# Kernel tuning notes

Measured on AMD Instinct MI355X. Metric: run time of the kernel, lower is better.

## Reference

```python
import jax, jax.numpy as jnp
import numpy as np

D_MODEL = 64
LN_EPS = 1e-5


def _conv1d(x, w, b, stride, pad):
    # x: (B, Cin, L), w: (Cout, Cin, K)
    y = jax.lax.conv_general_dilated(x, w, (stride,), [(pad, pad)],
                                     dimension_numbers=('NCH', 'OIH', 'NCH'))
    return y + b[None, :, None]


def _layernorm(x, g, b):
    # normalize over last dim (feature dim), matching nn.LayerNorm(d_model)
    m = jnp.mean(x, axis=-1, keepdims=True)
    v = jnp.var(x, axis=-1, keepdims=True)
    return (x - m) * jax.lax.rsqrt(v + LN_EPS) * g + b


def _pos_embed(L, d):
    pos = jnp.arange(L, dtype=jnp.float32)[:, None]
    div = jnp.exp(jnp.arange(0, d, 2, dtype=jnp.float32) * (-np.log(10000.0) / d))
    pe = jnp.zeros((L, d), jnp.float32)
    pe = pe.at[:, 0::2].set(jnp.sin(pos * div))
    pe = pe.at[:, 1::2].set(jnp.cos(pos * div))
    return pe


def setup_inputs():
    key = jax.random.key(0)
    ks = jax.random.split(key, 20)
    B, L, D = 128, 4096, D_MODEL
    G = D // 4  # 16 convs per kernel-size group (kernels cycle [3,5,7,9])
    inp = {'x': jax.random.normal(ks[0], (B, 1, L), jnp.float32)}
    kernels = [3, 5, 7, 9]
    for i, k in enumerate(kernels):
        fan = float(1.0 / np.sqrt(k))
        inp['tok_w%d' % k] = jax.random.uniform(ks[1 + 2 * i], (G, 1, k), jnp.float32, -fan, fan)
        inp['tok_b%d' % k] = jax.random.uniform(ks[2 + 2 * i], (G,), jnp.float32, -fan, fan)
    fan = float(1.0 / np.sqrt(D * 4))
    for j in range(3):
        inp['c_w%d' % (j + 1)] = jax.random.uniform(ks[10 + 2 * j], (D, D, 4), jnp.float32, -fan, fan)
        inp['c_b%d' % (j + 1)] = jax.random.uniform(ks[11 + 2 * j], (D,), jnp.float32, -fan, fan)
    for j in range(2):
        inp['ln_g%d' % (j + 1)] = jnp.ones((D,), jnp.float32)
        inp['ln_b%d' % (j + 1)] = jnp.zeros((D,), jnp.float32)
    return inp


def reference(x, tok_w3, tok_b3, tok_w5, tok_b5, tok_w7, tok_b7, tok_w9, tok_b9,
              c_w1, c_b1, c_w2, c_b2, c_w3, c_b3, ln_g1, ln_b1, ln_g2, ln_b2):
    B, _, L = x.shape
    D = D_MODEL
    # TokenEmbedding: conv i has kernel [3,5,7,9][i%4]; fuse the d_model 1-channel
    # convs into 4 grouped convs (one per kernel size), then interleave channels.
    outs = [
        _conv1d(x, tok_w3, tok_b3, 1, 1),
        _conv1d(x, tok_w5, tok_b5, 1, 2),
        _conv1d(x, tok_w7, tok_b7, 1, 3),
        _conv1d(x, tok_w9, tok_b9, 1, 4),
    ]  # each (B, D//4, L); group g holds channels i with i % 4 == g, ordered by i // 4
    emb = jnp.stack(outs, axis=2).reshape(B, D, L)  # channel i = (i//4)*4 + (i%4)
    # add sinusoidal positional embedding (dropout is identity in eval mode)
    h = emb + _pos_embed(L, D).T[None]  # (B, D, L)
    # CompressionEmbedding: conv(k=4, s=2, p=1) -> tanh -> LN (over D) chain
    h = jnp.tanh(_conv1d(h, c_w1, c_b1, 2, 1))
    h = _layernorm(h.transpose(0, 2, 1), ln_g1, ln_b1).transpose(0, 2, 1)
    h = jnp.tanh(_conv1d(h, c_w2, c_b2, 2, 1))
    h = _layernorm(h.transpose(0, 2, 1), ln_g2, ln_b2).transpose(0, 2, 1)
    h = jnp.tanh(_conv1d(h, c_w3, c_b3, 2, 1))
    return h.transpose(0, 2, 1)  # (B, L//8, D)
```

## Files before the change

kernel.cpp:

```cpp
#include <hip/hip_runtime.h>
#include <math.h>

#define BATCH 128
#define LN_EPS 1e-5f

typedef short bf16x8 __attribute__((ext_vector_type(8)));
typedef short bf16x4 __attribute__((ext_vector_type(4)));
typedef float f32x4  __attribute__((ext_vector_type(4)));

__device__ __forceinline__ ushort f2bf(float f) {
    return __builtin_bit_cast(ushort, (__bf16)f);
}

__device__ __forceinline__ float fast_tanh(float v) {
    float e = __expf(2.f * v);
    float r = __builtin_amdgcn_rcpf(e + 1.f);
    return fmaf(-2.f, r, 1.f);
}

__device__ __forceinline__ float fast_rsqrt(float v) {
    return __builtin_amdgcn_rsqf(v);
}

__global__ __launch_bounds__(256, 2)
void prep_kernel(const float* __restrict__ cw1, const float* __restrict__ cw2,
                 const float* __restrict__ cw3,
                 const float* __restrict__ w3, const float* __restrict__ b3,
                 const float* __restrict__ w5, const float* __restrict__ b5,
                 const float* __restrict__ w7, const float* __restrict__ b7,
                 const float* __restrict__ w9, const float* __restrict__ b9,
                 const float* __restrict__ cb1, const float* __restrict__ cb2,
                 const float* __restrict__ cb3,
                 const float* __restrict__ lg1, const float* __restrict__ lb1,
                 const float* __restrict__ lg2, const float* __restrict__ lb2,
                 ushort* __restrict__ Wm23, ushort* __restrict__ Wm1,
                 float* __restrict__ W0c, float* __restrict__ W3c,
                 float* __restrict__ pe1c,
                 float* __restrict__ cb2t, float* __restrict__ B2k0,
                 float* __restrict__ B2k3,
                 float* __restrict__ cb3t, float* __restrict__ B3k0,
                 float* __restrict__ B3k3) {
    const int tid = threadIdx.x;
    const int bx  = blockIdx.x;

    __shared__ float tile[64][12];
    __shared__ float red[4][64][24];

    if (tid < 64) {
        int idx = bx * 64 + tid;
        int s = idx >> 14, r = idx & 16383;
        int j = r & 7, l15 = (r >> 3) & 15, dt = (r >> 7) & 3;
        int quad = (r >> 9) & 3, k2 = (r >> 11) & 1, kk = (r >> 12) & 3;
        int dout = dt * 16 + l15, din = k2 * 32 + quad * 8 + j;
        const float* cw = (s == 0) ? cw2 : cw3;
        const float* lg = (s == 0) ? lg1 : lg2;
        Wm23[idx] = f2bf(cw[dout * 256 + din * 4 + kk] * lg[din]);
    }

    if (bx == 1 && tid < 128) {
        const int s = tid >> 6, ch = tid & 63;
        const float* cw = (s == 0) ? cw2 : cw3;
        const float* lb = (s == 0) ? lb1 : lb2;
        float full = 0.f, k0 = 0.f, k3 = 0.f;
        for (int din = 0; din < 64; ++din) {
            float bv = lb[din];
            const float* wr = cw + ch * 256 + din * 4;
            k0 = fmaf(wr[0], bv, k0);
            k3 = fmaf(wr[3], bv, k3);
            full = fmaf(wr[0] + wr[1] + wr[2] + wr[3], bv, full);
        }
        if (s == 0) { cb2t[ch] = cb2[ch] + full; B2k0[ch] = k0; B2k3[ch] = k3; }
        else        { cb3t[ch] = cb3[ch] + full; B3k0[ch] = k0; B3k3[ch] = k3; }
    }

    if (bx == 0) {
        const int ch = tid & 63, part = tid >> 6;
        const float* cw1row = cw1 + ch * 256;
        float acc[24];
#pragma unroll
        for (int j = 0; j < 24; ++j) acc[j] = 0.f;
        for (int din = part * 16; din < part * 16 + 16; ++din) {
            int ki = din & 3, g = din >> 2;
            float wl[9];
#pragma unroll
            for (int j = 0; j < 9; ++j) wl[j] = 0.f;
            if (ki == 0)      { for (int j = 0; j < 3; ++j) wl[3 + j] = w3[g * 3 + j]; }
            else if (ki == 1) { for (int j = 0; j < 5; ++j) wl[2 + j] = w5[g * 5 + j]; }
            else if (ki == 2) { for (int j = 0; j < 7; ++j) wl[1 + j] = w7[g * 7 + j]; }
            else              { for (int j = 0; j < 9; ++j) wl[j]     = w9[g * 9 + j]; }
#pragma unroll
            for (int kk = 0; kk < 4; ++kk) {
                float c = cw1row[din * 4 + kk];
#pragma unroll
                for (int u = 0; u < 9; ++u) acc[kk + u] += c * wl[u];
            }
            float c0 = cw1row[din * 4 + 0], c3 = cw1row[din * 4 + 3];
#pragma unroll
            for (int u = 0; u < 4; ++u) { acc[16 + u] += c0 * wl[5 + u]; acc[20 + u] += c3 * wl[u]; }
        }
#pragma unroll
        for (int j = 0; j < 24; ++j) red[part][ch][j] = acc[j];
    }

    for (int i = tid; i < 320; i += 256) {
        int d2 = i / 10, pp = i - d2 * 10;
        int p = 8 * bx - 1 + pp;
        int din0 = 2 * d2, g = d2 >> 1;
        float sv = 0.f, cv = 0.f;
        if (p >= 0 && p < 4096) {
            float dv = __expf((float)din0 * -0.14391156831212787f);
            float s, c;
            __sincosf((float)p * dv, &s, &c);
            bool lo = (din0 & 3) == 0;
            sv = s + (lo ? b3[g] : b7[g]);
            cv = c + (lo ? b5[g] : b9[g]);
        }
        tile[din0][pp] = sv;
        tile[din0 + 1][pp] = cv;
    }
    __syncthreads();

    if (bx == 0 && tid < 64) {
        const int ch = tid;
        float w24[24];
#pragma unroll
        for (int j = 0; j < 24; ++j)
            w24[j] = red[0][ch][j] + red[1][ch][j] + red[2][ch][j] + red[3][ch][j];
        int dt = ch >> 4, l15 = ch & 15;
#pragma unroll
        for (int quad = 0; quad < 4; ++quad)
#pragma unroll
            for (int j = 0; j < 8; ++j) {
                int k = quad * 8 + j;
                Wm1[((quad * 4 + dt) * 16 + l15) * 8 + j] = f2bf(k < 12 ? w24[k] : 0.f);
            }
#pragma unroll
        for (int u = 0; u < 4; ++u) { W0c[ch * 4 + u] = w24[16 + u]; W3c[ch * 4 + u] = w24[20 + u]; }
    }

    {
        const int ll = tid >> 6, ch = tid & 63;
        const int l = bx * 4 + ll;
        float acc = cb1[ch];
        const float* cwr = cw1 + ch * 256;
        for (int din = 0; din < 64; ++din) {
            float4 w = *(const float4*)(cwr + din * 4);
            acc = fmaf(w.x, tile[din][2 * ll + 0],
                  fmaf(w.y, tile[din][2 * ll + 1],
                  fmaf(w.z, tile[din][2 * ll + 2],
                  fmaf(w.w, tile[din][2 * ll + 3], acc))));
        }
        pe1c[(size_t)l * 64 + ch] = acc;
    }
}

__global__ __launch_bounds__(256, 2)
void mega_kernel(const float* __restrict__ x,
                 const ushort* __restrict__ Wm1, const ushort* __restrict__ Wm23,
                 const float* __restrict__ pe1c,
                 const float* __restrict__ W0c, const float* __restrict__ W3c,
                 const float* __restrict__ cb2t, const float* __restrict__ B2k0,
                 const float* __restrict__ B2k3,
                 const float* __restrict__ cb3t, const float* __restrict__ B3k0,
                 const float* __restrict__ B3k3,
                 float* __restrict__ out) {
    const int b0 = blockIdx.y;
    const int g0 = blockIdx.x * 32;
    const int tid = threadIdx.x;

    __shared__ __align__(16) ushort xs[2][320];
    __shared__ __align__(16) ushort TE1[2][68][72];
    __shared__ __align__(16) ushort TO1[2][68][72];
    __shared__ __align__(16) ushort TE2[2][34][72];
    __shared__ __align__(16) ushort TO2[2][34][72];

    for (int i = tid; i < 640; i += 256) {
        int ba = (i >= 320) ? 1 : 0, j = i - ba * 320;
        int g = 8 * g0 - 11 + j;
        float v = (g >= 0 && g < 4096) ? x[(size_t)(b0 + ba * 64) * 4096 + g] : 0.f;
        xs[ba][j] = f2bf(v);
    }
    __syncthreads();

    const int wv = tid >> 6, lane = tid & 63;
    const int quad = lane >> 4, l15 = lane & 15;

    {
        bf16x8 afr1[4];
#pragma unroll
        for (int dt = 0; dt < 4; ++dt)
            afr1[dt] = *(const bf16x8*)&Wm1[((quad * 4 + dt) * 16 + l15) * 8];
        const int qstart = 4 * g0 - 3;

        float4 pv[4];
        unsigned xA[4], xB[4];
        {
            const int m = wv * 16 + l15;
            const int q = qstart + m;
            const int qc = (q < 0) ? 0 : ((q > 2047) ? 2047 : q);
            const float* pb_ = pe1c + (size_t)qc * 64 + quad * 4;
#pragma unroll
            for (int dt = 0; dt < 4; ++dt) pv[dt] = *(const float4*)(pb_ + dt * 16);
            const unsigned* pA = (const unsigned*)&xs[0][2 * m + 8 * quad];
            const unsigned* pB = (const unsigned*)&xs[1][2 * m + 8 * quad];
#pragma unroll
            for (int i = 0; i < 4; ++i) { xA[i] = pA[i]; xB[i] = pB[i]; }
        }
        for (int pass = wv; pass < 9; pass += 4) {
            const int m = pass * 16 + l15;
            const int q = qstart + m;
            union { bf16x8 v; unsigned u[4]; } tA, tB;
#pragma unroll
            for (int i = 0; i < 4; ++i) { tA.u[i] = xA[i]; tB.u[i] = xB[i]; }
            f32x4 a1[2][4];
#pragma unroll
            for (int dt = 0; dt < 4; ++dt) {
                f32x4 c;
                c[0] = pv[dt].x; c[1] = pv[dt].y; c[2] = pv[dt].z; c[3] = pv[dt].w;
                a1[0][dt] = __builtin_amdgcn_mfma_f32_16x16x32_bf16(afr1[dt], tA.v, c, 0, 0, 0);
                a1[1][dt] = __builtin_amdgcn_mfma_f32_16x16x32_bf16(afr1[dt], tB.v, c, 0, 0, 0);
            }
            if (pass + 4 < 9) {
                const int m2 = m + 64;
                const int q2 = q + 64;
                const int qc2 = (q2 < 0) ? 0 : ((q2 > 2047) ? 2047 : q2);
                const float* pb2 = pe1c + (size_t)qc2 * 64 + quad * 4;
#pragma unroll
                for (int dt = 0; dt < 4; ++dt) pv[dt] = *(const float4*)(pb2 + dt * 16);
                const unsigned* pA2 = (const unsigned*)&xs[0][2 * m2 + 8 * quad];
                const unsigned* pB2 = (const unsigned*)&xs[1][2 * m2 + 8 * quad];
#pragma unroll
                for (int i = 0; i < 4; ++i) { xA[i] = pA2[i]; xB[i] = pB2[i]; }
            }
            if (m < 134) {
                ushort* dstA = (m & 1) ? &TE1[0][(m + 1) >> 1][0] : &TO1[0][m >> 1][0];
                ushort* dstB = (m & 1) ? &TE1[1][(m + 1) >> 1][0] : &TO1[1][m >> 1][0];
                if (q >= 0 && q < 2048) {
                    if (q == 0 || q == 2047) {
                        const float* Wc = (q == 0) ? W0c : W3c;
#pragma unroll
                        for (int ba = 0; ba < 2; ++ba) {
                            const float* xe = x + (size_t)(b0 + ba * 64) * 4096
                                                + ((q == 0) ? 0 : 4092);
                            float x0 = xe[0], x1 = xe[1], x2 = xe[2], x3 = xe[3];
#pragma unroll
                            for (int dt = 0; dt < 4; ++dt)
#pragma unroll
                                for (int r = 0; r < 4; ++r) {
                                    const float* wc = Wc + (dt * 16 + quad * 4 + r) * 4;
                                    a1[ba][dt][r] -= wc[0] * x0 + wc[1] * x1 + wc[2] * x2 + wc[3] * x3;
                                }
                        }
                    }
                    float vA[16], vB[16];
                    float sA = 0.f, s2A = 0.f, sB = 0.f, s2B = 0.f;
#pragma unroll
                    for (int dt = 0; dt < 4; ++dt)
#pragma unroll
                        for (int r = 0; r < 4; ++r) {
                            float ta = fast_tanh(a1[0][dt][r]);
                            float tb = fast_tanh(a1[1][dt][r]);
                            vA[dt * 4 + r] = ta; vB[dt * 4 + r] = tb;
                            sA += ta; s2A = fmaf(ta, ta, s2A);
                            sB += tb; s2B = fmaf(tb, tb, s2B);
                        }
                    sA += __shfl_xor(sA, 16, 64);  sB += __shfl_xor(sB, 16, 64);
                    s2A += __shfl_xor(s2A, 16, 64); s2B += __shfl_xor(s2B, 16, 64);
                    sA += __shfl_xor(sA, 32, 64);  sB += __shfl_xor(sB, 32, 64);
                    s2A += __shfl_xor(s2A, 32, 64); s2B += __shfl_xor(s2B, 32, 64);
                    float meanA = sA * 0.015625f, meanB = sB * 0.015625f;
                    float varA = fmaf(-meanA, meanA, s2A * 0.015625f);
                    float varB = fmaf(-meanB, meanB, s2B * 0.015625f);
                    float rstdA = fast_rsqrt(varA + LN_EPS), rstdB = fast_rsqrt(varB + LN_EPS);
                    float nmrA = -meanA * rstdA, nmrB = -meanB * rstdB;
#pragma unroll
                    for (int dt = 0; dt < 4; ++dt) {
                        bf16x4 pkA, pkB;
#pragma unroll
                        for (int r = 0; r < 4; ++r) {
                            pkA[r] = (short)f2bf(fmaf(vA[dt * 4 + r], rstdA, nmrA));
                            pkB[r] = (short)f2bf(fmaf(vB[dt * 4 + r], rstdB, nmrB));
                        }
                        *(bf16x4*)(dstA + dt * 16 + quad * 4) = pkA;
                        *(bf16x4*)(dstB + dt * 16 + quad * 4) = pkB;
                    }
                } else {
                    bf16x4 z; z[0] = 0; z[1] = 0; z[2] = 0; z[3] = 0;
#pragma unroll
                    for (int dt = 0; dt < 4; ++dt) {
                        *(bf16x4*)(dstA + dt * 16 + quad * 4) = z;
                        *(bf16x4*)(dstB + dt * 16 + quad * 4) = z;
                    }
                }
            }
        }
    }
    __syncthreads();

    {
        f32x4 cfr2[4];
#pragma unroll
        for (int dt = 0; dt < 4; ++dt) {
            float4 cv = *(const float4*)(cb2t + dt * 16 + quad * 4);
            cfr2[dt][0] = cv.x; cfr2[dt][1] = cv.y; cfr2[dt][2] = cv.z; cfr2[dt][3] = cv.w;
        }
        for (int pass = wv; pass < 5; pass += 4) {
            const int n = pass * 16 + l15;
            const int nc = (n < 66) ? n : 65;
            f32x4 a2[2][4];
#pragma unroll
            for (int dt = 0; dt < 4; ++dt) { a2[0][dt] = cfr2[dt]; a2[1][dt] = cfr2[dt]; }
#pragma unroll
            for (int kk = 0; kk < 4; ++kk) {
                const int row = nc + ((kk + 1) >> 1);
#pragma unroll
                for (int k2 = 0; k2 < 2; ++k2) {
                    bf16x8 bfrA = (kk & 1) ? *(const bf16x8*)&TE1[0][row][k2 * 32 + quad * 8]
                                           : *(const bf16x8*)&TO1[0][row][k2 * 32 + quad * 8];
                    bf16x8 bfrB = (kk & 1) ? *(const bf16x8*)&TE1[1][row][k2 * 32 + quad * 8]
                                           : *(const bf16x8*)&TO1[1][row][k2 * 32 + quad * 8];
                    const ushort* wb = Wm23 + ((((kk * 2 + k2) * 4 + quad) * 4) * 16) * 8;
#pragma unroll
                    for (int dt = 0; dt < 4; ++dt) {
                        bf16x8 afr = *(const bf16x8*)(wb + ((size_t)(dt * 16 + l15)) * 8);
                        a2[0][dt] = __builtin_amdgcn_mfma_f32_16x16x32_bf16(afr, bfrA, a2[0][dt], 0, 0, 0);
                        a2[1][dt] = __builtin_amdgcn_mfma_f32_16x16x32_bf16(afr, bfrB, a2[1][dt], 0, 0, 0);
                    }
                }
            }
            if (n < 66) {
                const int p = 2 * g0 - 1 + n;
                ushort* dstA = (n & 1) ? &TE2[0][(n + 1) >> 1][0] : &TO2[0][n >> 1][0];
                ushort* dstB = (n & 1) ? &TE2[1][(n + 1) >> 1][0] : &TO2[1][n >> 1][0];
                if (p >= 0 && p < 1024) {
                    if (p == 0 || p == 1023) {
                        const float* Bc = (p == 0) ? B2k0 : B2k3;
#pragma unroll
                        for (int dt = 0; dt < 4; ++dt)
#pragma unroll
                            for (int r = 0; r < 4; ++r) {
                                float bc = Bc[dt * 16 + quad * 4 + r];
                                a2[0][dt][r] -= bc;
                                a2[1][dt][r] -= bc;
                            }
                    }
                    float vA[16], vB[16];
                    float sA = 0.f, s2A = 0.f, sB = 0.f, s2B = 0.f;
#pragma unroll
                    for (int dt = 0; dt < 4; ++dt)
#pragma unroll
                        for (int r = 0; r < 4; ++r) {
                            float ta = fast_tanh(a2[0][dt][r]);
                            float tb = fast_tanh(a2[1][dt][r]);
                            vA[dt * 4 + r] = ta; vB[dt * 4 + r] = tb;
                            sA += ta; s2A = fmaf(ta, ta, s2A);
                            sB += tb; s2B = fmaf(tb, tb, s2B);
                        }
                    sA += __shfl_xor(sA, 16, 64);  sB += __shfl_xor(sB, 16, 64);
                    s2A += __shfl_xor(s2A, 16, 64); s2B += __shfl_xor(s2B, 16, 64);
                    sA += __shfl_xor(sA, 32, 64);  sB += __shfl_xor(sB, 32, 64);
                    s2A += __shfl_xor(s2A, 32, 64); s2B += __shfl_xor(s2B, 32, 64);
                    float meanA = sA * 0.015625f, meanB = sB * 0.015625f;
                    float varA = fmaf(-meanA, meanA, s2A * 0.015625f);
                    float varB = fmaf(-meanB, meanB, s2B * 0.015625f);
                    float rstdA = fast_rsqrt(varA + LN_EPS), rstdB = fast_rsqrt(varB + LN_EPS);
                    float nmrA = -meanA * rstdA, nmrB = -meanB * rstdB;
#pragma unroll
                    for (int dt = 0; dt < 4; ++dt) {
                        bf16x4 pkA, pkB;
#pragma unroll
                        for (int r = 0; r < 4; ++r) {
                            pkA[r] = (short)f2bf(fmaf(vA[dt * 4 + r], rstdA, nmrA));
                            pkB[r] = (short)f2bf(fmaf(vB[dt * 4 + r], rstdB, nmrB));
                        }
                        *(bf16x4*)(dstA + dt * 16 + quad * 4) = pkA;
                        *(bf16x4*)(dstB + dt * 16 + quad * 4) = pkB;
                    }
                } else {
                    bf16x4 z; z[0] = 0; z[1] = 0; z[2] = 0; z[3] = 0;
#pragma unroll
                    for (int dt = 0; dt < 4; ++dt) {
                        *(bf16x4*)(dstA + dt * 16 + quad * 4) = z;
                        *(bf16x4*)(dstB + dt * 16 + quad * 4) = z;
                    }
                }
            }
        }
    }
    __syncthreads();

    {
        const int m3 = (wv & 1) * 16 + l15;
        const int dth = wv >> 1;
        f32x4 a3[2][2];
#pragma unroll
        for (int d2 = 0; d2 < 2; ++d2) {
            float4 cv = *(const float4*)(cb3t + (dth * 2 + d2) * 16 + quad * 4);
            f32x4 c; c[0] = cv.x; c[1] = cv.y; c[2] = cv.z; c[3] = cv.w;
            a3[0][d2] = c; a3[1][d2] = c;
        }
        const ushort* Wg3 = Wm23 + 16384;
#pragma unroll
        for (int kk = 0; kk < 4; ++kk) {
            const int row = m3 + ((kk + 1) >> 1);
#pragma unroll
            for (int k2 = 0; k2 < 2; ++k2) {
                bf16x8 bfrA = (kk & 1) ? *(const bf16x8*)&TE2[0][row][k2 * 32 + quad * 8]
                                       : *(const bf16x8*)&TO2[0][row][k2 * 32 + quad * 8];
                bf16x8 bfrB = (kk & 1) ? *(const bf16x8*)&TE2[1][row][k2 * 32 + quad * 8]
                                       : *(const bf16x8*)&TO2[1][row][k2 * 32 + quad * 8];
                const ushort* wb = Wg3 + ((((kk * 2 + k2) * 4 + quad) * 4) * 16) * 8;
#pragma unroll
                for (int d2 = 0; d2 < 2; ++d2) {
                    const int dt = dth * 2 + d2;
                    bf16x8 afr = *(const bf16x8*)(wb + ((size_t)(dt * 16 + l15)) * 8);
                    a3[0][d2] = __builtin_amdgcn_mfma_f32_16x16x32_bf16(afr, bfrA, a3[0][d2], 0, 0, 0);
                    a3[1][d2] = __builtin_amdgcn_mfma_f32_16x16x32_bf16(afr, bfrB, a3[1][d2], 0, 0, 0);
                }
            }
        }
        const int l = g0 + m3;
        if (l == 0 || l == 511) {
            const float* Bc = (l == 0) ? B3k0 : B3k3;
#pragma unroll
            for (int ba = 0; ba < 2; ++ba)
#pragma unroll
                for (int d2 = 0; d2 < 2; ++d2)
#pragma unroll
                    for (int r = 0; r < 4; ++r)
                        a3[ba][d2][r] -= Bc[(dth * 2 + d2) * 16 + quad * 4 + r];
        }
#pragma unroll
        for (int ba = 0; ba < 2; ++ba) {
            float* ob = out + ((size_t)((b0 + ba * 64) * 512) + l) * 64;
#pragma unroll
            for (int d2 = 0; d2 < 2; ++d2) {
                const int dt = dth * 2 + d2;
                float4 st = make_float4(fast_tanh(a3[ba][d2][0]),
                                        fast_tanh(a3[ba][d2][1]),
                                        fast_tanh(a3[ba][d2][2]),
                                        fast_tanh(a3[ba][d2][3]));
                *(float4*)(ob + dt * 16 + quad * 4) = st;
            }
        }
    }
}

extern "C" void kernel_launch(void* const* d_in, const int* in_sizes, int n_in,
                              void* d_out, int out_size, void* d_ws, size_t ws_size,
                              hipStream_t stream) {
    (void)in_sizes; (void)n_in; (void)out_size; (void)ws_size;
    const float* x   = (const float*)d_in[0];
    const float* w3  = (const float*)d_in[1];
    const float* b3  = (const float*)d_in[2];
    const float* w5  = (const float*)d_in[3];
    const float* b5  = (const float*)d_in[4];
    const float* w7  = (const float*)d_in[5];
    const float* b7  = (const float*)d_in[6];
    const float* w9  = (const float*)d_in[7];
    const float* b9  = (const float*)d_in[8];
    const float* cw1 = (const float*)d_in[9];
    const float* cb1 = (const float*)d_in[10];
    const float* cw2 = (const float*)d_in[11];
    const float* cb2 = (const float*)d_in[12];
    const float* cw3 = (const float*)d_in[13];
    const float* cb3 = (const float*)d_in[14];
    const float* lg1 = (const float*)d_in[15];
    const float* lb1 = (const float*)d_in[16];
    const float* lg2 = (const float*)d_in[17];
    const float* lb2 = (const float*)d_in[18];
    float* out = (float*)d_out;

    char* w = (char*)d_ws;
    ushort* Wm23 = (ushort*)(w + 0);
    ushort* Wm1  = (ushort*)(w + 65536);
    float*  W0c  = (float*)(w + 69632);
    float*  W3c  = (float*)(w + 70656);
    float*  cb2t = (float*)(w + 71680);
    float*  B2k0 = (float*)(w + 71936);
    float*  B2k3 = (float*)(w + 72192);
    float*  cb3t = (float*)(w + 72448);
    float*  B3k0 = (float*)(w + 72704);
    float*  B3k3 = (float*)(w + 72960);
    float*  pe1c = (float*)(w + 73216);

    prep_kernel<<<512, 256, 0, stream>>>(cw1, cw2, cw3, w3, b3, w5, b5, w7, b7, w9, b9,
                                         cb1, cb2, cb3, lg1, lb1, lg2, lb2,
                                         Wm23, Wm1, W0c, W3c, pe1c,
                                         cb2t, B2k0, B2k3, cb3t, B3k0, B3k3);
    mega_kernel<<<dim3(16, BATCH / 2), 256, 0, stream>>>(
        x, Wm1, Wm23, pe1c, W0c, W3c, cb2t, B2k0, B2k3, cb3t, B3k0, B3k3, out);
}
```

Measured before the change: 143.2 us.

## Split fused mega kernel into separate stage-1 and stage-2/3 kernels via global buffer

```diff
diff --git a/kernel.cpp b/kernel.cpp
--- a/kernel.cpp
+++ b/kernel.cpp
@@ -155,147 +155,126 @@
 }
 
 __global__ __launch_bounds__(256, 2)
-void mega_kernel(const float* __restrict__ x,
-                 const ushort* __restrict__ Wm1, const ushort* __restrict__ Wm23,
-                 const float* __restrict__ pe1c,
-                 const float* __restrict__ W0c, const float* __restrict__ W3c,
-                 const float* __restrict__ cb2t, const float* __restrict__ B2k0,
-                 const float* __restrict__ B2k3,
-                 const float* __restrict__ cb3t, const float* __restrict__ B3k0,
-                 const float* __restrict__ B3k3,
-                 float* __restrict__ out) {
+void stage1_kernel(const float* __restrict__ x, const ushort* __restrict__ Wm1,
+                   const float* __restrict__ pe1c,
+                   const float* __restrict__ W0c, const float* __restrict__ W3c,
+                   ushort* __restrict__ h1) {
+    const int b = blockIdx.y;
+    const int q0 = blockIdx.x * 64;
+    const int tid = threadIdx.x;
+
+    __shared__ __align__(16) ushort xs[160];
+
+    for (int i = tid; i < 160; i += 256) {
+        int g = 2 * q0 - 5 + i;
+        float v = (g >= 0 && g < 4096) ? x[(size_t)b * 4096 + g] : 0.f;
+        xs[i] = f2bf(v);
+    }
+    __syncthreads();
+
+    const int wv = tid >> 6, lane = tid & 63;
+    const int quad = lane >> 4, l15 = lane & 15;
+    const int m = wv * 16 + l15;
+    const int q = q0 + m;
+
+    bf16x8 afr1[4];
+#pragma unroll
+    for (int dt = 0; dt < 4; ++dt)
+        afr1[dt] = *(const bf16x8*)&Wm1[((quad * 4 + dt) * 16 + l15) * 8];
+
+    f32x4 a1[4];
+    {
+        const float* pb_ = pe1c + (size_t)q * 64 + quad * 4;
+#pragma unroll
+        for (int dt = 0; dt < 4; ++dt) {
+            float4 pv = *(const float4*)(pb_ + dt * 16);
+            a1[dt][0] = pv.x; a1[dt][1] = pv.y; a1[dt][2] = pv.z; a1[dt][3] = pv.w;
+        }
+    }
+    union { bf16x8 v; unsigned u[4]; } tmp;
+    {
+        const unsigned* p = (const unsigned*)&xs[2 * m + 8 * quad];
+#pragma unroll
+        for (int i = 0; i < 4; ++i) tmp.u[i] = p[i];
+    }
+#pragma unroll
+    for (int dt = 0; dt < 4; ++dt)
+        a1[dt] = __builtin_amdgcn_mfma_f32_16x16x32_bf16(afr1[dt], tmp.v, a1[dt], 0, 0, 0);
+
+    if (q == 0 || q == 2047) {
+        const float* Wc = (q == 0) ? W0c : W3c;
+        const float* xe = x + (size_t)b * 4096 + ((q == 0) ? 0 : 4092);
+        float x0 = xe[0], x1 = xe[1], x2 = xe[2], x3 = xe[3];
+#pragma unroll
+        for (int dt = 0; dt < 4; ++dt)
+#pragma unroll
+            for (int r = 0; r < 4; ++r) {
+                const float* wc = Wc + (dt * 16 + quad * 4 + r) * 4;
+                a1[dt][r] -= wc[0] * x0 + wc[1] * x1 + wc[2] * x2 + wc[3] * x3;
+            }
+    }
+    float v[16], s = 0.f, s2 = 0.f;
+#pragma unroll
+    for (int dt = 0; dt < 4; ++dt)
+#pragma unroll
+        for (int r = 0; r < 4; ++r) {
+            float t = fast_tanh(a1[dt][r]);
+            v[dt * 4 + r] = t;
+            s += t;
+            s2 = fmaf(t, t, s2);
+        }
+    s += __shfl_xor(s, 16, 64);
+    s += __shfl_xor(s, 32, 64);
+    s2 += __shfl_xor(s2, 16, 64);
+    s2 += __shfl_xor(s2, 32, 64);
+    float mean = s * 0.015625f;
+    float var = fmaf(-mean, mean, s2 * 0.015625f);
+    float rstd = fast_rsqrt(var + LN_EPS);
+    float nmr = -mean * rstd;
+    ushort* hb = h1 + ((size_t)b * 2048 + q) * 64;
+#pragma unroll
+    for (int dt = 0; dt < 4; ++dt) {
+        bf16x4 pk;
+#pragma unroll
+        for (int r = 0; r < 4; ++r)
+            pk[r] = (short)f2bf(fmaf(v[dt * 4 + r], rstd, nmr));
+        *(bf16x4*)(hb + dt * 16 + quad * 4) = pk;
+    }
+}
+
+__global__ __launch_bounds__(256, 2)
+void stage23_kernel(const ushort* __restrict__ h1, const ushort* __restrict__ Wm23,
+                    const float* __restrict__ cb2t, const float* __restrict__ B2k0,
+                    const float* __restrict__ B2k3,
+                    const float* __restrict__ cb3t, const float* __restrict__ B3k0,
+                    const float* __restrict__ B3k3,
+                    float* __restrict__ out) {
     const int b0 = blockIdx.y;
     const int g0 = blockIdx.x * 32;
     const int tid = threadIdx.x;
 
-    __shared__ __align__(16) ushort xs[2][320];
     __shared__ __align__(16) ushort TE1[2][68][72];
     __shared__ __align__(16) ushort TO1[2][68][72];
     __shared__ __align__(16) ushort TE2[2][34][72];
     __shared__ __align__(16) ushort TO2[2][34][72];
 
-    for (int i = tid; i < 640; i += 256) {
-        int ba = (i >= 320) ? 1 : 0, j = i - ba * 320;
-        int g = 8 * g0 - 11 + j;
-        float v = (g >= 0 && g < 4096) ? x[(size_t)(b0 + ba * 64) * 4096 + g] : 0.f;
-        xs[ba][j] = f2bf(v);
+    for (int i = tid; i < 2 * 136 * 16; i += 256) {
+        int ba = i / 2176, rem = i - ba * 2176;
+        int row = rem >> 4, piece = rem & 15;
+        ushort* dst;
+        int q;
+        if (row < 68) { dst = &TE1[ba][row][piece * 4];      q = 4 * g0 + 2 * row - 4; }
+        else          { int r2 = row - 68;
+                        dst = &TO1[ba][r2][piece * 4];       q = 4 * g0 + 2 * r2 - 3; }
+        unsigned long long v = 0ull;
+        if (q >= 0 && q < 2048)
+            v = *(const unsigned long long*)&h1[((size_t)(b0 + ba * 64) * 2048 + q) * 64 + piece * 4];
+        *(unsigned long long*)dst = v;
     }
     __syncthreads();
 
     const int wv = tid >> 6, lane = tid & 63;
     const int quad = lane >> 4, l15 = lane & 15;
-
-    {
-        bf16x8 afr1[4];
-#pragma unroll
-        for (int dt = 0; dt < 4; ++dt)
-            afr1[dt] = *(const bf16x8*)&Wm1[((quad * 4 + dt) * 16 + l15) * 8];
-        const int qstart = 4 * g0 - 3;
-
-        float4 pv[4];
-        unsigned xA[4], xB[4];
-        {
-            const int m = wv * 16 + l15;
-            const int q = qstart + m;
-            const int qc = (q < 0) ? 0 : ((q > 2047) ? 2047 : q);
-            const float* pb_ = pe1c + (size_t)qc * 64 + quad * 4;
-#pragma unroll
-            for (int dt = 0; dt < 4; ++dt) pv[dt] = *(const float4*)(pb_ + dt * 16);
-            const unsigned* pA = (const unsigned*)&xs[0][2 * m + 8 * quad];
-            const unsigned* pB = (const unsigned*)&xs[1][2 * m + 8 * quad];
-#pragma unroll
-            for (int i = 0; i < 4; ++i) { xA[i] = pA[i]; xB[i] = pB[i]; }
-        }
-        for (int pass = wv; pass < 9; pass += 4) {
-            const int m = pass * 16 + l15;
-            const int q = qstart + m;
-            union { bf16x8 v; unsigned u[4]; } tA, tB;
-#pragma unroll
-            for (int i = 0; i < 4; ++i) { tA.u[i] = xA[i]; tB.u[i] = xB[i]; }
-            f32x4 a1[2][4];
-#pragma unroll
-            for (int dt = 0; dt < 4; ++dt) {
-                f32x4 c;
-                c[0] = pv[dt].x; c[1] = pv[dt].y; c[2] = pv[dt].z; c[3] = pv[dt].w;
-                a1[0][dt] = __builtin_amdgcn_mfma_f32_16x16x32_bf16(afr1[dt], tA.v, c, 0, 0, 0);
-                a1[1][dt] = __builtin_amdgcn_mfma_f32_16x16x32_bf16(afr1[dt], tB.v, c, 0, 0, 0);
-            }
-            if (pass + 4 < 9) {
-                const int m2 = m + 64;
-                const int q2 = q + 64;
-                const int qc2 = (q2 < 0) ? 0 : ((q2 > 2047) ? 2047 : q2);
-                const float* pb2 = pe1c + (size_t)qc2 * 64 + quad * 4;
-#pragma unroll
-                for (int dt = 0; dt < 4; ++dt) pv[dt] = *(const float4*)(pb2 + dt * 16);
-                const unsigned* pA2 = (const unsigned*)&xs[0][2 * m2 + 8 * quad];
-                const unsigned* pB2 = (const unsigned*)&xs[1][2 * m2 + 8 * quad];
-#pragma unroll
-                for (int i = 0; i < 4; ++i) { xA[i] = pA2[i]; xB[i] = pB2[i]; }
-            }
-            if (m < 134) {
-                ushort* dstA = (m & 1) ? &TE1[0][(m + 1) >> 1][0] : &TO1[0][m >> 1][0];
-                ushort* dstB = (m & 1) ? &TE1[1][(m + 1) >> 1][0] : &TO1[1][m >> 1][0];
-                if (q >= 0 && q < 2048) {
-                    if (q == 0 || q == 2047) {
-                        const float* Wc = (q == 0) ? W0c : W3c;
-#pragma unroll
-                        for (int ba = 0; ba < 2; ++ba) {
-                            const float* xe = x + (size_t)(b0 + ba * 64) * 4096
-                                                + ((q == 0) ? 0 : 4092);
-                            float x0 = xe[0], x1 = xe[1], x2 = xe[2], x3 = xe[3];
-#pragma unroll
-                            for (int dt = 0; dt < 4; ++dt)
-#pragma unroll
-                                for (int r = 0; r < 4; ++r) {
-                                    const float* wc = Wc + (dt * 16 + quad * 4 + r) * 4;
-                                    a1[ba][dt][r] -= wc[0] * x0 + wc[1] * x1 + wc[2] * x2 + wc[3] * x3;
-                                }
-                        }
-                    }
-                    float vA[16], vB[16];
-                    float sA = 0.f, s2A = 0.f, sB = 0.f, s2B = 0.f;
-#pragma unroll
-                    for (int dt = 0; dt < 4; ++dt)
-#pragma unroll
-                        for (int r = 0; r < 4; ++r) {
-                            float ta = fast_tanh(a1[0][dt][r]);
-                            float tb = fast_tanh(a1[1][dt][r]);
-                            vA[dt * 4 + r] = ta; vB[dt * 4 + r] = tb;
-                            sA += ta; s2A = fmaf(ta, ta, s2A);
-                            sB += tb; s2B = fmaf(tb, tb, s2B);
-                        }
-                    sA += __shfl_xor(sA, 16, 64);  sB += __shfl_xor(sB, 16, 64);
-                    s2A += __shfl_xor(s2A, 16, 64); s2B += __shfl_xor(s2B, 16, 64);
-                    sA += __shfl_xor(sA, 32, 64);  sB += __shfl_xor(sB, 32, 64);
-                    s2A += __shfl_xor(s2A, 32, 64); s2B += __shfl_xor(s2B, 32, 64);
-                    float meanA = sA * 0.015625f, meanB = sB * 0.015625f;
-                    float varA = fmaf(-meanA, meanA, s2A * 0.015625f);
-                    float varB = fmaf(-meanB, meanB, s2B * 0.015625f);
-                    float rstdA = fast_rsqrt(varA + LN_EPS), rstdB = fast_rsqrt(varB + LN_EPS);
-                    float nmrA = -meanA * rstdA, nmrB = -meanB * rstdB;
-#pragma unroll
-                    for (int dt = 0; dt < 4; ++dt) {
-                        bf16x4 pkA, pkB;
-#pragma unroll
-                        for (int r = 0; r < 4; ++r) {
-                            pkA[r] = (short)f2bf(fmaf(vA[dt * 4 + r], rstdA, nmrA));
-                            pkB[r] = (short)f2bf(fmaf(vB[dt * 4 + r], rstdB, nmrB));
-                        }
-                        *(bf16x4*)(dstA + dt * 16 + quad * 4) = pkA;
-                        *(bf16x4*)(dstB + dt * 16 + quad * 4) = pkB;
-                    }
-                } else {
-                    bf16x4 z; z[0] = 0; z[1] = 0; z[2] = 0; z[3] = 0;
-#pragma unroll
-                    for (int dt = 0; dt < 4; ++dt) {
-                        *(bf16x4*)(dstA + dt * 16 + quad * 4) = z;
-                        *(bf16x4*)(dstB + dt * 16 + quad * 4) = z;
-                    }
-                }
-            }
-        }
-    }
-    __syncthreads();
 
     {
         f32x4 cfr2[4];
@@ -483,11 +462,13 @@
     float*  B3k0 = (float*)(w + 72704);
     float*  B3k3 = (float*)(w + 72960);
     float*  pe1c = (float*)(w + 73216);
+    ushort* h1   = (ushort*)(w + 1048576);
 
     prep_kernel<<<512, 256, 0, stream>>>(cw1, cw2, cw3, w3, b3, w5, b5, w7, b7, w9, b9,
                                          cb1, cb2, cb3, lg1, lb1, lg2, lb2,
                                          Wm23, Wm1, W0c, W3c, pe1c,
                                          cb2t, B2k0, B2k3, cb3t, B3k0, B3k3);
-    mega_kernel<<<dim3(16, BATCH / 2), 256, 0, stream>>>(
-        x, Wm1, Wm23, pe1c, W0c, W3c, cb2t, B2k0, B2k3, cb3t, B3k0, B3k3, out);
-}
+    stage1_kernel<<<dim3(32, BATCH), 256, 0, stream>>>(x, Wm1, pe1c, W0c, W3c, h1);
+    stage23_kernel<<<dim3(16, BATCH / 2), 256, 0, stream>>>(
+        h1, Wm23, cb2t, B2k0, B2k3, cb3t, B3k0, B3k3, out);
+}
```

New measurement: 166.8 us. 16.5% more time.
